# Performance work log

Measured on AMD Instinct MI355X. Metric: run time of the kernel, lower is better.

## Reference

```python
import jax, jax.numpy as jnp
import numpy as np

D_MODEL = 1024
N_HEADS = 16
D_K = D_MODEL // N_HEADS

def _xavier(key, shape):
    fan_in, fan_out = shape[1], shape[0]
    limit = float(np.sqrt(6.0 / (fan_in + fan_out)))
    return jax.random.uniform(key, shape, jnp.float32, -limit, limit)

def setup_inputs() -> dict:
    key = jax.random.key(0)
    ks = jax.random.split(key, 7)
    B, S = 2, 2048
    return {
        "query": jax.random.normal(ks[0], (B, S, D_MODEL), jnp.float32),
        "key": jax.random.normal(ks[1], (B, S, D_MODEL), jnp.float32),
        "value": jax.random.normal(ks[2], (B, S, D_MODEL), jnp.float32),
        "w_q": _xavier(ks[3], (D_MODEL, D_MODEL)),  # torch Linear weight [out, in]
        "w_k": _xavier(ks[4], (D_MODEL, D_MODEL)),
        "w_v": _xavier(ks[5], (D_MODEL, D_MODEL)),
        "w_o": _xavier(ks[6], (D_MODEL, D_MODEL)),
        "ln_gamma": jnp.ones((D_MODEL,), jnp.float32),
        "ln_beta": jnp.zeros((D_MODEL,), jnp.float32),
    }

def reference(query, key, value, w_q, w_k, w_v, w_o, ln_gamma, ln_beta):
    B, S, _ = query.shape
    # projections (torch Linear: x @ W.T), split into heads -> [B, H, S, d_k]
    def split_heads(x, W):
        return (x @ W.T).reshape(B, S, N_HEADS, D_K).transpose(0, 2, 1, 3)
    Q = split_heads(query, w_q)
    K = split_heads(key, w_k)
    V = split_heads(value, w_v)
    scores = jnp.einsum('bhqd,bhkd->bhqk', Q, K) / jnp.sqrt(jnp.float32(D_K))
    attn = jax.nn.softmax(scores, axis=-1)  # dropout disabled (p=0 / eval)
    ctx = jnp.einsum('bhqk,bhkd->bhqd', attn, V)
    ctx = ctx.transpose(0, 2, 1, 3).reshape(B, S, D_MODEL)
    out = ctx @ w_o.T
    # residual + LayerNorm
    x = query + out
    mu = jnp.mean(x, axis=-1, keepdims=True)
    var = jnp.var(x, axis=-1, keepdims=True)
    return (x - mu) / jnp.sqrt(var + 1e-5) * ln_gamma + ln_beta
```

## Files before the change

### kernel.cpp

```cpp
#include <hip/hip_runtime.h>
#include <hip/hip_bf16.h>

#define DEVI __device__ __forceinline__

typedef float f32x4 __attribute__((ext_vector_type(4)));
typedef short bf16x8 __attribute__((ext_vector_type(8)));
typedef unsigned short ushort_t;

DEVI ushort_t f2bf(float x) {
  union { float f; unsigned u; } c; c.f = x;
  unsigned u = c.u;
  unsigned r = (u + 0x7fffu + ((u >> 16) & 1u)) >> 16;
  return (ushort_t)r;
}

DEVI float bf2f(unsigned hw) {
  union { unsigned u; float f; } c; c.u = hw << 16; return c.f;
}

DEVI unsigned cvt_pk_bf16(float lo, float hi) {
  unsigned r;
  asm volatile("v_cvt_pk_bf16_f32 %0, %1, %2" : "=v"(r) : "v"(lo), "v"(hi));
  return r;
}

DEVI void gload16(const ushort_t* g, ushort_t* l) {
  __builtin_amdgcn_global_load_lds(
      (const __attribute__((address_space(1))) unsigned int*)g,
      (__attribute__((address_space(3))) unsigned int*)l, 16, 0, 0);
}

#define WAITL0() asm volatile("s_waitcnt lgkmcnt(0)" ::: "memory")


__global__ __launch_bounds__(256)
void cvtN_kernel(const float* __restrict__ p0, const float* __restrict__ p1,
                 const float* __restrict__ p2, const float* __restrict__ p3,
                 ushort_t* __restrict__ o0, ushort_t* __restrict__ o1,
                 ushort_t* __restrict__ o2, ushort_t* __restrict__ o3, int n8) {
  int z = blockIdx.y;
  const float* in = (z == 0) ? p0 : (z == 1) ? p1 : (z == 2) ? p2 : p3;
  ushort_t* out = (z == 0) ? o0 : (z == 1) ? o1 : (z == 2) ? o2 : o3;
  int i = blockIdx.x * 256 + threadIdx.x;
  if (i >= n8) return;
  const float4* p = (const float4*)in + (size_t)i * 2;
  float4 a = p[0], b = p[1];
  uint4 v;
  v.x = cvt_pk_bf16(a.x, a.y);
  v.y = cvt_pk_bf16(a.z, a.w);
  v.z = cvt_pk_bf16(b.x, b.y);
  v.w = cvt_pk_bf16(b.z, b.w);
  ((uint4*)out)[i] = v;
}


__global__ __launch_bounds__(256)
void gemm128(const ushort_t* __restrict__ A0, const ushort_t* __restrict__ A1,
             const ushort_t* __restrict__ A2,
             const ushort_t* __restrict__ W0, const ushort_t* __restrict__ W1,
             const ushort_t* __restrict__ W2,
             void* __restrict__ O0, void* __restrict__ O1,
             void* __restrict__ O2, int mode_base, int nsteps, float qscale) {
  constexpr int K = 1024;
  int z = blockIdx.z;
  int mode = (mode_base == 3) ? 3 : mode_base + z;
  const ushort_t* A = (z == 0) ? A0 : (z == 1) ? A1 : A2;
  const ushort_t* W = (z == 0) ? W0 : (z == 1) ? W1 : W2;
  void* Op = (z == 0) ? O0 : (z == 1) ? O1 : O2;
  if (mode == 3) {
    A = A0 + z * 512;
    W = W0 + z * 512;
    Op = z ? O1 : O0;
  }
  float scale = (mode == 0) ? qscale : 1.0f;
  int m0 = (mode == 2) ? blockIdx.x * 128 : blockIdx.y * 128;
  int n0 = (mode == 2) ? blockIdx.y * 128 : blockIdx.x * 128;

  __shared__ __align__(16) ushort_t Asm[2][128 * 64];
  __shared__ __align__(16) ushort_t Bsm[2][128 * 64];

  int t = threadIdx.x;
  int lane = t & 63, wave = t >> 6;
  int wm = wave >> 1, wn = wave & 1;
  int col = lane & 15, g = lane >> 4;
  int lr = lane >> 3, lc = lane & 7;
  int cswz = col & 7;

  const ushort_t* aSrc = A + (size_t)(m0 + wave * 32 + lr) * K + (lc ^ lr) * 8;
  const ushort_t* bSrc = W + (size_t)(n0 + wave * 32 + lr) * K + (lc ^ lr) * 8;

  f32x4 z4 = {0.f, 0.f, 0.f, 0.f};
  f32x4 acc[4][4];
  for (int i = 0; i < 4; i++)
    for (int j = 0; j < 4; j++) acc[i][j] = z4;

#define GEMM_STAGE(buf, koff) do {                                         \
    _Pragma("unroll")                                                      \
    for (int i_ = 0; i_ < 4; i_++) {                                       \
      gload16(aSrc + (koff) + i_ * 8 * K,                                  \
              &Asm[buf][(wave * 32 + i_ * 8) * 64]);                       \
      gload16(bSrc + (koff) + i_ * 8 * K,                                  \
              &Bsm[buf][(wave * 32 + i_ * 8) * 64]);                       \
    }                                                                      \
  } while (0)

  GEMM_STAGE(0, 0);
  __syncthreads();

  for (int kt = 0; kt < nsteps; ++kt) {
    int cur = kt & 1;
    if (kt < nsteps - 1) GEMM_STAGE(cur ^ 1, (kt + 1) * 64);
    const ushort_t* As = Asm[cur];
    const ushort_t* Bs = Bsm[cur];
#pragma unroll
    for (int kk = 0; kk < 2; ++kk) {
      bf16x8 af[4], bfr[4];
#pragma unroll
      for (int mi = 0; mi < 4; mi++) {
        int row = wm * 64 + mi * 16 + col;
        af[mi] = *(const bf16x8*)(As + row * 64 + (((kk * 4 + g) ^ cswz) * 8));
      }
#pragma unroll
      for (int ni = 0; ni < 4; ni++) {
        int row = wn * 64 + ni * 16 + col;
        bfr[ni] = *(const bf16x8*)(Bs + row * 64 + (((kk * 4 + g) ^ cswz) * 8));
      }
      __builtin_amdgcn_s_setprio(1);
#pragma unroll
      for (int mi = 0; mi < 4; mi++)
#pragma unroll
        for (int ni = 0; ni < 4; ni++)
          acc[mi][ni] = __builtin_amdgcn_mfma_f32_16x16x32_bf16(af[mi], bfr[ni],
                                                                acc[mi][ni], 0, 0, 0);
      __builtin_amdgcn_s_setprio(0);
    }
    __syncthreads();
  }

#pragma unroll
  for (int mi = 0; mi < 4; mi++)
#pragma unroll
    for (int ni = 0; ni < 4; ni++)
#pragma unroll
      for (int r = 0; r < 4; r++) {
        int m = m0 + wm * 64 + mi * 16 + g * 4 + r;
        int n = n0 + wn * 64 + ni * 16 + col;
        float v = acc[mi][ni][r] * scale;
        if (mode <= 1) {
          int b = m >> 11, s = m & 2047, h = n >> 6, d = n & 63;
          ((ushort_t*)Op)[(((size_t)(b * 16 + h) * 2048 + s) * 64) + d] = f2bf(v);
        } else if (mode == 2) {
          int h = m >> 6, d = m & 63, b = n >> 11, s = n & 2047;
          ((ushort_t*)Op)[(((size_t)(b * 16 + h) * 64 + d) * 2048) + s] = f2bf(v);
        } else {
          ((ushort_t*)Op)[(size_t)m * 1024 + n] = f2bf(v);
        }
      }
#undef GEMM_STAGE
}


__global__ __launch_bounds__(256, 3)
void attn_kernel(const ushort_t* __restrict__ Qh, const ushort_t* __restrict__ Kh,
                 const ushort_t* __restrict__ Vt, ushort_t* __restrict__ ctx) {
  int qt = blockIdx.x;
  int bh = blockIdx.y;
  int t = threadIdx.x, lane = t & 63, wave = t >> 6;
  int col = lane & 15, g = lane >> 4;
  int lr = lane >> 3, lc = lane & 7;
  int cswz = col & 7;
  int q0 = qt * 128 + wave * 32;

  const ushort_t* Qp = Qh + (size_t)bh * 2048 * 64;
  const ushort_t* Kp = Kh + (size_t)bh * 2048 * 64;
  const ushort_t* Vp = Vt + (size_t)bh * 64 * 2048;

  __shared__ __align__(16) ushort_t Ksm[2][64 * 64];
  __shared__ __align__(16) ushort_t Vsm[2][64 * 64];
  __shared__ __align__(16) ushort_t Psm[4][2][16 * 64];

  const ushort_t* kSrc = Kp + (size_t)(wave * 16 + lr) * 64 + (lc ^ lr) * 8;
  const ushort_t* vSrc = Vp + (size_t)(wave * 16 + lr) * 2048 + (lc ^ lr) * 8;
  ushort_t* PsA = &Psm[wave][0][0];
  ushort_t* PsB = &Psm[wave][1][0];

#define ATTN_STAGE(buf, k0) do { \
    gload16(kSrc + (size_t)(k0) * 64,       &Ksm[buf][wave * 1024]);       \
    gload16(kSrc + (size_t)(k0) * 64 + 512, &Ksm[buf][wave * 1024 + 512]); \
    gload16(vSrc + (k0),                    &Vsm[buf][wave * 1024]);       \
    gload16(vSrc + (k0) + 16384,            &Vsm[buf][wave * 1024 + 512]); \
  } while (0)

  bf16x8 qa0 = *(const bf16x8*)(Qp + (size_t)(q0 + col) * 64 + g * 8);
  bf16x8 qa1 = *(const bf16x8*)(Qp + (size_t)(q0 + col) * 64 + 32 + g * 8);
  bf16x8 qb0 = *(const bf16x8*)(Qp + (size_t)(q0 + 16 + col) * 64 + g * 8);
  bf16x8 qb1 = *(const bf16x8*)(Qp + (size_t)(q0 + 16 + col) * 64 + 32 + g * 8);

  f32x4 z4 = {0.f, 0.f, 0.f, 0.f};
  f32x4 oa[4], ob[4];
  for (int i = 0; i < 4; i++) { oa[i] = z4; ob[i] = z4; }
  f32x4 la = z4, lb = z4;

  ATTN_STAGE(0, 0);
  __syncthreads();

  for (int it = 0; it < 32; ++it) {
    int cur = it & 1;
    if (it < 31) ATTN_STAGE(cur ^ 1, (it + 1) * 64);

    const ushort_t* Ks = Ksm[cur];
    const ushort_t* Vs = Vsm[cur];

    f32x4 sa[4], sb[4];
#pragma unroll
    for (int kt = 0; kt < 4; kt++) {
      int off = (kt * 16 + col) * 64 + ((g ^ cswz) * 8);
      bf16x8 kf0 = *(const bf16x8*)(Ks + off);
      bf16x8 kf1 = *(const bf16x8*)(Ks + (off ^ 32));
      f32x4 a = z4, b = z4;
      __builtin_amdgcn_s_setprio(1);
      a = __builtin_amdgcn_mfma_f32_16x16x32_bf16(kf0, qa0, a, 0, 0, 0);
      a = __builtin_amdgcn_mfma_f32_16x16x32_bf16(kf1, qa1, a, 0, 0, 0);
      b = __builtin_amdgcn_mfma_f32_16x16x32_bf16(kf0, qb0, b, 0, 0, 0);
      b = __builtin_amdgcn_mfma_f32_16x16x32_bf16(kf1, qb1, b, 0, 0, 0);
      __builtin_amdgcn_s_setprio(0);
      sa[kt] = a; sb[kt] = b;
    }

#pragma unroll
    for (int kt = 0; kt < 4; kt++) {
      float a0 = __builtin_amdgcn_exp2f(sa[kt][0]);
      float a1 = __builtin_amdgcn_exp2f(sa[kt][1]);
      float a2 = __builtin_amdgcn_exp2f(sa[kt][2]);
      float a3 = __builtin_amdgcn_exp2f(sa[kt][3]);
      la[0] += a0; la[1] += a1; la[2] += a2; la[3] += a3;
      uint2 pka;
      pka.x = cvt_pk_bf16(a0, a1);
      pka.y = cvt_pk_bf16(a2, a3);
      int pw = col * 64 + (((2 * kt + (g >> 1)) ^ cswz) * 8) + (g & 1) * 4;
      *(uint2*)(PsA + pw) = pka;
      float b0 = __builtin_amdgcn_exp2f(sb[kt][0]);
      float b1 = __builtin_amdgcn_exp2f(sb[kt][1]);
      float b2 = __builtin_amdgcn_exp2f(sb[kt][2]);
      float b3 = __builtin_amdgcn_exp2f(sb[kt][3]);
      lb[0] += b0; lb[1] += b1; lb[2] += b2; lb[3] += b3;
      uint2 pkb;
      pkb.x = cvt_pk_bf16(b0, b1);
      pkb.y = cvt_pk_bf16(b2, b3);
      *(uint2*)(PsB + pw) = pkb;
    }

    WAITL0();
    __builtin_amdgcn_sched_barrier(0);

#pragma unroll
    for (int kk = 0; kk < 2; kk++) {
      int po = col * 64 + (((kk * 4 + g) ^ cswz) * 8);
      bf16x8 pfa = *(const bf16x8*)(PsA + po);
      bf16x8 pfb = *(const bf16x8*)(PsB + po);
      __builtin_amdgcn_s_setprio(1);
#pragma unroll
      for (int dt = 0; dt < 4; dt++) {
        bf16x8 vf = *(const bf16x8*)(Vs + (dt * 16 + col) * 64 +
                                     (((kk * 4 + g) ^ cswz) * 8));
        oa[dt] = __builtin_amdgcn_mfma_f32_16x16x32_bf16(vf, pfa, oa[dt], 0, 0, 0);
        ob[dt] = __builtin_amdgcn_mfma_f32_16x16x32_bf16(vf, pfb, ob[dt], 0, 0, 0);
      }
      __builtin_amdgcn_s_setprio(0);
    }
    __syncthreads();
  }
#undef ATTN_STAGE

  float lva = (la[0] + la[1]) + (la[2] + la[3]);
  lva += __shfl_xor(lva, 16);
  lva += __shfl_xor(lva, 32);
  float lvb = (lb[0] + lb[1]) + (lb[2] + lb[3]);
  lvb += __shfl_xor(lvb, 16);
  lvb += __shfl_xor(lvb, 32);
  float inva = 1.0f / lva, invb = 1.0f / lvb;
  int b = bh >> 4, h = bh & 15;
#pragma unroll
  for (int dt = 0; dt < 4; dt++)
#pragma unroll
    for (int r = 0; r < 4; r++) {
      int d = dt * 16 + g * 4 + r;
      ctx[((size_t)(b * 2048 + q0 + col)) * 1024 + h * 64 + d] =
          f2bf(oa[dt][r] * inva);
      ctx[((size_t)(b * 2048 + q0 + 16 + col)) * 1024 + h * 64 + d] =
          f2bf(ob[dt][r] * invb);
    }
}


__global__ __launch_bounds__(256)
void ln_kernel(const float* __restrict__ resid, const ushort_t* __restrict__ p0,
               const ushort_t* __restrict__ p1,
               const float* __restrict__ gamma, const float* __restrict__ beta,
               float* __restrict__ out) {
  int m = blockIdx.x;
  int t = threadIdx.x;
  int lane = t & 63, wave = t >> 6;
  float4 a = ((const float4*)(resid + (size_t)m * 1024))[t];
  uint2 v0 = ((const uint2*)(p0 + (size_t)m * 1024))[t];
  uint2 v1 = ((const uint2*)(p1 + (size_t)m * 1024))[t];
  float4 x;
  x.x = a.x + bf2f(v0.x & 0xffffu) + bf2f(v1.x & 0xffffu);
  x.y = a.y + bf2f(v0.x >> 16)     + bf2f(v1.x >> 16);
  x.z = a.z + bf2f(v0.y & 0xffffu) + bf2f(v1.y & 0xffffu);
  x.w = a.w + bf2f(v0.y >> 16)     + bf2f(v1.y >> 16);
  float sum = (x.x + x.y) + (x.z + x.w);
  float ssq = x.x * x.x + x.y * x.y + x.z * x.z + x.w * x.w;
  for (int off = 1; off < 64; off <<= 1) {
    sum += __shfl_xor(sum, off);
    ssq += __shfl_xor(ssq, off);
  }
  __shared__ float red[8];
  if (lane == 0) { red[wave] = sum; red[4 + wave] = ssq; }
  __syncthreads();
  sum = red[0] + red[1] + red[2] + red[3];
  ssq = red[4] + red[5] + red[6] + red[7];
  float mu = sum * (1.f / 1024.f);
  float var = ssq * (1.f / 1024.f) - mu * mu;
  float rstd = rsqrtf(var + 1e-5f);
  const float4* gp = (const float4*)gamma;
  const float4* bp = (const float4*)beta;
  float4 gg = gp[t], bb = bp[t];
  float4 y;
  y.x = (x.x - mu) * rstd * gg.x + bb.x;
  y.y = (x.y - mu) * rstd * gg.y + bb.y;
  y.z = (x.z - mu) * rstd * gg.z + bb.z;
  y.w = (x.w - mu) * rstd * gg.w + bb.w;
  ((float4*)(out + (size_t)m * 1024))[t] = y;
}


extern "C" void kernel_launch(void* const* d_in, const int* in_sizes, int n_in,
                              void* d_out, int out_size, void* d_ws, size_t ws_size,
                              hipStream_t stream) {
  (void)in_sizes; (void)n_in; (void)out_size; (void)ws_size;
  const float* query = (const float*)d_in[0];
  const float* keyi  = (const float*)d_in[1];
  const float* value = (const float*)d_in[2];
  const float* w_q = (const float*)d_in[3];
  const float* w_k = (const float*)d_in[4];
  const float* w_v = (const float*)d_in[5];
  const float* w_o = (const float*)d_in[6];
  const float* ln_g = (const float*)d_in[7];
  const float* ln_b = (const float*)d_in[8];

  char* ws = (char*)d_ws;
  const size_t MB = 1u << 20;
  ushort_t* proj0 = (ushort_t*)(ws + 0 * MB);
  ushort_t* proj1 = (ushort_t*)(ws + 8 * MB);
  ushort_t* Xq  = (ushort_t*)(ws + 0 * MB);
  ushort_t* Xk  = (ushort_t*)(ws + 8 * MB);
  ushort_t* Xv  = (ushort_t*)(ws + 16 * MB);
  ushort_t* Wq  = (ushort_t*)(ws + 24 * MB);
  ushort_t* Wk  = (ushort_t*)(ws + 26 * MB);
  ushort_t* Wv  = (ushort_t*)(ws + 28 * MB);
  ushort_t* Wo  = (ushort_t*)(ws + 30 * MB);
  ushort_t* Qh  = (ushort_t*)(ws + 32 * MB);
  ushort_t* Kh  = (ushort_t*)(ws + 40 * MB);
  ushort_t* Vt  = (ushort_t*)(ws + 48 * MB);
  ushort_t* ctx = (ushort_t*)(ws + 56 * MB);

  const float SCL = 0.18033688f;

  cvtN_kernel<<<dim3(2048, 3), 256, 0, stream>>>(query, keyi, value, value,
                                                 Xq, Xk, Xv, Xv, 524288);
  cvtN_kernel<<<dim3(512, 4), 256, 0, stream>>>(w_q, w_k, w_v, w_o,
                                                Wq, Wk, Wv, Wo, 131072);

  gemm128<<<dim3(8, 32, 3), 256, 0, stream>>>(Xq, Xk, Wv, Wq, Wk, Xv,
                                              Qh, Kh, Vt, 0, 16, SCL);
  attn_kernel<<<dim3(16, 32), 256, 0, stream>>>(Qh, Kh, Vt, ctx);
  gemm128<<<dim3(8, 32, 2), 256, 0, stream>>>(ctx, ctx, ctx, Wo, Wo, Wo,
                                              proj0, proj1, proj0, 3, 8, 1.0f);
  ln_kernel<<<4096, 256, 0, stream>>>(query, proj0, proj1, ln_g, ln_b,
                                      (float*)d_out);
}
```

Baseline: 143.4 us.

## Fuse fp32-to-bf16 activation conversion into projection GEMM loads

Removes the separate conversion kernel for query/key/value and has the QKV projection GEMM read fp32 activations directly. The data goes through registers, is converted to bf16 with packed converts, and is written swizzled into shared memory after the MFMA work of each step, so the loads overlap compute. This drops one launch and a 24 MB write plus read-back of bf16 copies. In exchange the GEMM reads twice the bytes per tile, no longer uses async LDS loads on the fp32 side, and needs more registers to hold the staged data.

```diff
diff --git a/kernel.cpp b/kernel.cpp
--- a/kernel.cpp
+++ b/kernel.cpp
@@ -55,23 +55,23 @@
 
 
 __global__ __launch_bounds__(256)
-void gemm128(const ushort_t* __restrict__ A0, const ushort_t* __restrict__ A1,
-             const ushort_t* __restrict__ A2,
-             const ushort_t* __restrict__ W0, const ushort_t* __restrict__ W1,
-             const ushort_t* __restrict__ W2,
+void gemm128(const void* A0v, const void* A1v, const void* A2v,
+             const void* W0v, const void* W1v, const void* W2v,
              void* __restrict__ O0, void* __restrict__ O1,
              void* __restrict__ O2, int mode_base, int nsteps, float qscale) {
   constexpr int K = 1024;
   int z = blockIdx.z;
   int mode = (mode_base == 3) ? 3 : mode_base + z;
-  const ushort_t* A = (z == 0) ? A0 : (z == 1) ? A1 : A2;
-  const ushort_t* W = (z == 0) ? W0 : (z == 1) ? W1 : W2;
+  const void* Av = (z == 0) ? A0v : (z == 1) ? A1v : A2v;
+  const void* Wv = (z == 0) ? W0v : (z == 1) ? W1v : W2v;
   void* Op = (z == 0) ? O0 : (z == 1) ? O1 : O2;
   if (mode == 3) {
-    A = A0 + z * 512;
-    W = W0 + z * 512;
+    Av = (const ushort_t*)A0v + z * 512;
+    Wv = (const ushort_t*)W0v + z * 512;
     Op = z ? O1 : O0;
   }
+  bool aF32 = (mode <= 1);
+  bool bF32 = (mode == 2);
   float scale = (mode == 0) ? qscale : 1.0f;
   int m0 = (mode == 2) ? blockIdx.x * 128 : blockIdx.y * 128;
   int n0 = (mode == 2) ? blockIdx.y * 128 : blockIdx.x * 128;
@@ -86,30 +86,67 @@
   int lr = lane >> 3, lc = lane & 7;
   int cswz = col & 7;
 
-  const ushort_t* aSrc = A + (size_t)(m0 + wave * 32 + lr) * K + (lc ^ lr) * 8;
-  const ushort_t* bSrc = W + (size_t)(n0 + wave * 32 + lr) * K + (lc ^ lr) * 8;
+  const ushort_t* aSrcB =
+      (const ushort_t*)Av + (size_t)(m0 + wave * 32 + lr) * K + (lc ^ lr) * 8;
+  const ushort_t* bSrcB =
+      (const ushort_t*)Wv + (size_t)(n0 + wave * 32 + lr) * K + (lc ^ lr) * 8;
+  const float* aSrcF =
+      (const float*)Av + (size_t)(m0 + wave * 32 + lr) * K + lc * 8;
+  const float* bSrcF =
+      (const float*)Wv + (size_t)(n0 + wave * 32 + lr) * K + lc * 8;
 
   f32x4 z4 = {0.f, 0.f, 0.f, 0.f};
   f32x4 acc[4][4];
   for (int i = 0; i < 4; i++)
     for (int j = 0; j < 4; j++) acc[i][j] = z4;
 
-#define GEMM_STAGE(buf, koff) do {                                         \
+  float4 frA[4][2], frB[4][2];
+
+#define STAGE_B16(srcB, buf, arr, koff) do {                               \
+    _Pragma("unroll")                                                      \
+    for (int i_ = 0; i_ < 4; i_++)                                         \
+      gload16((srcB) + (koff) + i_ * 8 * K,                                \
+              &arr[buf][(wave * 32 + i_ * 8) * 64]);                       \
+  } while (0)
+
+#define F32_LOAD(srcF, koff, fr) do {                                      \
     _Pragma("unroll")                                                      \
     for (int i_ = 0; i_ < 4; i_++) {                                       \
-      gload16(aSrc + (koff) + i_ * 8 * K,                                  \
-              &Asm[buf][(wave * 32 + i_ * 8) * 64]);                       \
-      gload16(bSrc + (koff) + i_ * 8 * K,                                  \
-              &Bsm[buf][(wave * 32 + i_ * 8) * 64]);                       \
+      const float* p_ = (srcF) + (size_t)(i_ * 8) * K + (koff);            \
+      fr[i_][0] = *(const float4*)p_;                                      \
+      fr[i_][1] = *(const float4*)(p_ + 4);                                \
     }                                                                      \
   } while (0)
 
-  GEMM_STAGE(0, 0);
+#define F32_WRITE(buf, arr, fr) do {                                       \
+    _Pragma("unroll")                                                      \
+    for (int i_ = 0; i_ < 4; i_++) {                                       \
+      uint4 w_;                                                            \
+      w_.x = cvt_pk_bf16(fr[i_][0].x, fr[i_][0].y);                        \
+      w_.y = cvt_pk_bf16(fr[i_][0].z, fr[i_][0].w);                        \
+      w_.z = cvt_pk_bf16(fr[i_][1].x, fr[i_][1].y);                        \
+      w_.w = cvt_pk_bf16(fr[i_][1].z, fr[i_][1].w);                        \
+      *(uint4*)(&arr[buf][(wave * 32 + i_ * 8 + lr) * 64 + (lc ^ lr) * 8]) \
+          = w_;                                                            \
+    }                                                                      \
+  } while (0)
+
+  if (aF32) { F32_LOAD(aSrcF, 0, frA); } else { STAGE_B16(aSrcB, 0, Asm, 0); }
+  if (bF32) { F32_LOAD(bSrcF, 0, frB); } else { STAGE_B16(bSrcB, 0, Bsm, 0); }
+  if (aF32) F32_WRITE(0, Asm, frA);
+  if (bF32) F32_WRITE(0, Bsm, frB);
   __syncthreads();
 
   for (int kt = 0; kt < nsteps; ++kt) {
     int cur = kt & 1;
-    if (kt < nsteps - 1) GEMM_STAGE(cur ^ 1, (kt + 1) * 64);
+    bool pre = (kt < nsteps - 1);
+    if (pre) {
+      int koff = (kt + 1) * 64;
+      if (aF32) { F32_LOAD(aSrcF, koff, frA); }
+      else      { STAGE_B16(aSrcB, cur ^ 1, Asm, koff); }
+      if (bF32) { F32_LOAD(bSrcF, koff, frB); }
+      else      { STAGE_B16(bSrcB, cur ^ 1, Bsm, koff); }
+    }
     const ushort_t* As = Asm[cur];
     const ushort_t* Bs = Bsm[cur];
 #pragma unroll
@@ -133,6 +170,10 @@
           acc[mi][ni] = __builtin_amdgcn_mfma_f32_16x16x32_bf16(af[mi], bfr[ni],
                                                                 acc[mi][ni], 0, 0, 0);
       __builtin_amdgcn_s_setprio(0);
+    }
+    if (pre) {
+      if (aF32) F32_WRITE(cur ^ 1, Asm, frA);
+      if (bF32) F32_WRITE(cur ^ 1, Bsm, frB);
     }
     __syncthreads();
   }
@@ -156,7 +197,9 @@
           ((ushort_t*)Op)[(size_t)m * 1024 + n] = f2bf(v);
         }
       }
-#undef GEMM_STAGE
+#undef STAGE_B16
+#undef F32_LOAD
+#undef F32_WRITE
 }
 
 
@@ -353,9 +396,6 @@
   const size_t MB = 1u << 20;
   ushort_t* proj0 = (ushort_t*)(ws + 0 * MB);
   ushort_t* proj1 = (ushort_t*)(ws + 8 * MB);
-  ushort_t* Xq  = (ushort_t*)(ws + 0 * MB);
-  ushort_t* Xk  = (ushort_t*)(ws + 8 * MB);
-  ushort_t* Xv  = (ushort_t*)(ws + 16 * MB);
   ushort_t* Wq  = (ushort_t*)(ws + 24 * MB);
   ushort_t* Wk  = (ushort_t*)(ws + 26 * MB);
   ushort_t* Wv  = (ushort_t*)(ws + 28 * MB);
@@ -367,12 +407,11 @@
 
   const float SCL = 0.18033688f;
 
-  cvtN_kernel<<<dim3(2048, 3), 256, 0, stream>>>(query, keyi, value, value,
-                                                 Xq, Xk, Xv, Xv, 524288);
   cvtN_kernel<<<dim3(512, 4), 256, 0, stream>>>(w_q, w_k, w_v, w_o,
                                                 Wq, Wk, Wv, Wo, 131072);
 
-  gemm128<<<dim3(8, 32, 3), 256, 0, stream>>>(Xq, Xk, Wv, Wq, Wk, Xv,
+  gemm128<<<dim3(8, 32, 3), 256, 0, stream>>>(query, keyi, Wv,
+                                              Wq, Wk, value,
                                               Qh, Kh, Vt, 0, 16, SCL);
   attn_kernel<<<dim3(16, 32), 256, 0, stream>>>(Qh, Kh, Vt, ctx);
   gemm128<<<dim3(8, 32, 2), 256, 0, stream>>>(ctx, ctx, ctx, Wo, Wo, Wo,
```

Measured after the change: 158.1 us. +10.2%, slower.

## Keep softmax probabilities in registers by permuting key rows at load time

Applied to the files above, without the earlier changes.

Key rows are loaded into shared memory in a permuted order, so the QK^T MFMA output layout of each lane lines up with the B-operand layout of the PV MFMA. The exponentiated scores can then be packed straight into registers instead of going through a per-wave shared-memory P buffer. This removes the LDS writes, the wait and the LDS reads for P, and frees shared memory, so the occupancy hint goes from 3 to 4 blocks. The key permutation must match the V column ordering exactly or the results will be wrong, and the higher occupancy target may force register spills.

```diff
diff --git a/kernel.cpp b/kernel.cpp
--- a/kernel.cpp
+++ b/kernel.cpp
@@ -160,7 +160,7 @@
 }
 
 
-__global__ __launch_bounds__(256, 3)
+__global__ __launch_bounds__(256, 4)
 void attn_kernel(const ushort_t* __restrict__ Qh, const ushort_t* __restrict__ Kh,
                  const ushort_t* __restrict__ Vt, ushort_t* __restrict__ ctx) {
   int qt = blockIdx.x;
@@ -177,18 +177,21 @@
 
   __shared__ __align__(16) ushort_t Ksm[2][64 * 64];
   __shared__ __align__(16) ushort_t Vsm[2][64 * 64];
-  __shared__ __align__(16) ushort_t Psm[4][2][16 * 64];
-
-  const ushort_t* kSrc = Kp + (size_t)(wave * 16 + lr) * 64 + (lc ^ lr) * 8;
+
+  int slot0 = wave * 16 + lr;
+  int slot1 = slot0 + 8;
+  int key0 = (slot0 & 0x20) | ((slot0 & 0x0C) << 1) | ((slot0 & 0x10) >> 2) | (slot0 & 3);
+  int key1 = (slot1 & 0x20) | ((slot1 & 0x0C) << 1) | ((slot1 & 0x10) >> 2) | (slot1 & 3);
+
+  const ushort_t* kSrc0 = Kp + (size_t)key0 * 64 + (lc ^ lr) * 8;
+  const ushort_t* kSrc1 = Kp + (size_t)key1 * 64 + (lc ^ lr) * 8;
   const ushort_t* vSrc = Vp + (size_t)(wave * 16 + lr) * 2048 + (lc ^ lr) * 8;
-  ushort_t* PsA = &Psm[wave][0][0];
-  ushort_t* PsB = &Psm[wave][1][0];
 
 #define ATTN_STAGE(buf, k0) do { \
-    gload16(kSrc + (size_t)(k0) * 64,       &Ksm[buf][wave * 1024]);       \
-    gload16(kSrc + (size_t)(k0) * 64 + 512, &Ksm[buf][wave * 1024 + 512]); \
-    gload16(vSrc + (k0),                    &Vsm[buf][wave * 1024]);       \
-    gload16(vSrc + (k0) + 16384,            &Vsm[buf][wave * 1024 + 512]); \
+    gload16(kSrc0 + (size_t)(k0) * 64, &Ksm[buf][wave * 1024]);        \
+    gload16(kSrc1 + (size_t)(k0) * 64, &Ksm[buf][wave * 1024 + 512]);  \
+    gload16(vSrc + (k0),               &Vsm[buf][wave * 1024]);        \
+    gload16(vSrc + (k0) + 16384,       &Vsm[buf][wave * 1024 + 512]);  \
   } while (0)
 
   bf16x8 qa0 = *(const bf16x8*)(Qp + (size_t)(q0 + col) * 64 + g * 8);
@@ -227,6 +230,7 @@
       sa[kt] = a; sb[kt] = b;
     }
 
+    unsigned pka[8], pkb[8];
 #pragma unroll
     for (int kt = 0; kt < 4; kt++) {
       float a0 = __builtin_amdgcn_exp2f(sa[kt][0]);
@@ -234,37 +238,31 @@
       float a2 = __builtin_amdgcn_exp2f(sa[kt][2]);
       float a3 = __builtin_amdgcn_exp2f(sa[kt][3]);
       la[0] += a0; la[1] += a1; la[2] += a2; la[3] += a3;
-      uint2 pka;
-      pka.x = cvt_pk_bf16(a0, a1);
-      pka.y = cvt_pk_bf16(a2, a3);
-      int pw = col * 64 + (((2 * kt + (g >> 1)) ^ cswz) * 8) + (g & 1) * 4;
-      *(uint2*)(PsA + pw) = pka;
+      pka[2 * kt]     = cvt_pk_bf16(a0, a1);
+      pka[2 * kt + 1] = cvt_pk_bf16(a2, a3);
       float b0 = __builtin_amdgcn_exp2f(sb[kt][0]);
       float b1 = __builtin_amdgcn_exp2f(sb[kt][1]);
       float b2 = __builtin_amdgcn_exp2f(sb[kt][2]);
       float b3 = __builtin_amdgcn_exp2f(sb[kt][3]);
       lb[0] += b0; lb[1] += b1; lb[2] += b2; lb[3] += b3;
-      uint2 pkb;
-      pkb.x = cvt_pk_bf16(b0, b1);
-      pkb.y = cvt_pk_bf16(b2, b3);
-      *(uint2*)(PsB + pw) = pkb;
-    }
-
-    WAITL0();
-    __builtin_amdgcn_sched_barrier(0);
+      pkb[2 * kt]     = cvt_pk_bf16(b0, b1);
+      pkb[2 * kt + 1] = cvt_pk_bf16(b2, b3);
+    }
 
 #pragma unroll
     for (int kk = 0; kk < 2; kk++) {
-      int po = col * 64 + (((kk * 4 + g) ^ cswz) * 8);
-      bf16x8 pfa = *(const bf16x8*)(PsA + po);
-      bf16x8 pfb = *(const bf16x8*)(PsB + po);
+      union { uint4 u; bf16x8 f; } ua, ub;
+      ua.u.x = pka[4 * kk];     ua.u.y = pka[4 * kk + 1];
+      ua.u.z = pka[4 * kk + 2]; ua.u.w = pka[4 * kk + 3];
+      ub.u.x = pkb[4 * kk];     ub.u.y = pkb[4 * kk + 1];
+      ub.u.z = pkb[4 * kk + 2]; ub.u.w = pkb[4 * kk + 3];
       __builtin_amdgcn_s_setprio(1);
 #pragma unroll
       for (int dt = 0; dt < 4; dt++) {
         bf16x8 vf = *(const bf16x8*)(Vs + (dt * 16 + col) * 64 +
                                      (((kk * 4 + g) ^ cswz) * 8));
-        oa[dt] = __builtin_amdgcn_mfma_f32_16x16x32_bf16(vf, pfa, oa[dt], 0, 0, 0);
-        ob[dt] = __builtin_amdgcn_mfma_f32_16x16x32_bf16(vf, pfb, ob[dt], 0, 0, 0);
+        oa[dt] = __builtin_amdgcn_mfma_f32_16x16x32_bf16(vf, ua.f, oa[dt], 0, 0, 0);
+        ob[dt] = __builtin_amdgcn_mfma_f32_16x16x32_bf16(vf, ub.f, ob[dt], 0, 0, 0);
       }
       __builtin_amdgcn_s_setprio(0);
     }
```

Result: faster. 140.2 us (-2.2%).
